# Kernel optimization log

Hardware: AMD Instinct MI355X
Metric: run time of the kernel (lower is better)

## Reference

```python
import jax, jax.numpy as jnp
import numpy as np

DIM = 512
HEADS = 16
HEAD_DIM = DIM // HEADS
WH, WW = 7, 7
N = WH * WW
OUP = 512
SCALE = HEAD_DIM ** -0.5
NW = 64  # windows per image (mask leading dim)


def _relative_position_index():
    coords = np.stack(np.meshgrid(np.arange(WH), np.arange(WW), indexing='ij'))  # (2,Wh,Ww)
    flat = coords.reshape(2, -1)                           # (2, N)
    rel = flat[:, :, None] - flat[:, None, :]              # (2, N, N)
    rel = rel.transpose(1, 2, 0).astype(np.int64)          # (N, N, 2)
    rel[:, :, 0] += WH - 1
    rel[:, :, 1] += WW - 1
    rel[:, :, 0] *= 2 * WW - 1
    return jnp.asarray(rel.sum(-1))                        # (N, N) int

REL_IDX = _relative_position_index()


def setup_inputs() -> dict:
    key = jax.random.key(0)
    ks = jax.random.split(key, 8)
    B_ = 4096
    x = jax.random.normal(ks[0], (B_, N, DIM), dtype=jnp.float32)
    mask = jnp.zeros((NW, N, N), dtype=jnp.float32)
    qkv_w = jax.random.normal(ks[1], (3 * DIM, DIM), dtype=jnp.float32) * (DIM ** -0.5)
    qkv_b = jax.random.normal(ks[2], (3 * DIM,), dtype=jnp.float32) * 0.02
    table = jax.random.normal(ks[3], ((2 * WH - 1) * (2 * WW - 1), HEADS), dtype=jnp.float32) * 0.02
    proj_w = jax.random.normal(ks[4], (OUP, DIM), dtype=jnp.float32) * (DIM ** -0.5)
    proj_b = jax.random.normal(ks[5], (OUP,), dtype=jnp.float32) * 0.02
    return {"x": x, "mask": mask, "qkv_w": qkv_w, "qkv_b": qkv_b,
            "table": table, "proj_w": proj_w, "proj_b": proj_b}


def reference(x, mask, qkv_w, qkv_b, table, proj_w, proj_b):
    B_, n, c = x.shape
    qkv = x @ qkv_w.T + qkv_b                               # (B_, N, 3C)
    qkv = qkv.reshape(B_, n, 3, HEADS, HEAD_DIM).transpose(2, 0, 3, 1, 4)
    q, k, v = qkv[0], qkv[1], qkv[2]                        # (B_, H, N, hd)
    q = q * SCALE
    attn = jnp.einsum('bhnd,bhmd->bhnm', q, k)              # (B_, H, N, N)
    bias = table[REL_IDX]                                   # (N, N, H) gather
    attn = attn + bias.transpose(2, 0, 1)[None]             # add rel-pos bias
    nW = mask.shape[0]
    attn = attn.reshape(B_ // nW, nW, HEADS, n, n) + mask[None, :, None]
    attn = attn.reshape(B_, HEADS, n, n)
    attn = jax.nn.softmax(attn, axis=-1)
    out = jnp.einsum('bhnm,bhmd->bhnd', attn, v)            # (B_, H, N, hd)
    out = out.transpose(0, 2, 1, 3).reshape(B_, n, c)
    return out @ proj_w.T + proj_b
```

## Files before the change

kernel.cpp:

```cpp
#include <hip/hip_runtime.h>
#include <hip/hip_bf16.h>
#include <stdint.h>

#define DIMC 512
#define HEADS 16
#define HEAD_DIM 32
#define NTOK 49
#define SCALE 0.17677669529663687f

typedef unsigned short u16;
typedef short bf16x8 __attribute__((ext_vector_type(8)));
typedef float f32x4 __attribute__((ext_vector_type(4)));
typedef u16 u16x8 __attribute__((ext_vector_type(8)));

#define MFMA16(a, b, c) __builtin_amdgcn_mfma_f32_16x16x32_bf16((a), (b), (c), 0, 0, 0)

__device__ __forceinline__ u16 f2bf(float f) {
  __hip_bfloat16 h = __float2bfloat16(f);
  u16 u;
  __builtin_memcpy(&u, &h, 2);
  return u;
}

__device__ __forceinline__ void gld16(const void* g, void* l) {
  __builtin_amdgcn_global_load_lds(
      (const __attribute__((address_space(1))) uint32_t*)g,
      (__attribute__((address_space(3))) uint32_t*)l, 16, 0, 0);
}

__global__ void cvt_f32_bf16(const float* __restrict__ in, u16* __restrict__ out, int n) {
  const int stride = gridDim.x * blockDim.x;
  for (int i = blockIdx.x * blockDim.x + threadIdx.x; i * 8 < n; i += stride) {
    const float4 v0 = ((const float4*)(in + i * 8))[0];
    const float4 v1 = ((const float4*)(in + i * 8))[1];
    u16x8 r;
    r[0] = f2bf(v0.x); r[1] = f2bf(v0.y); r[2] = f2bf(v0.z); r[3] = f2bf(v0.w);
    r[4] = f2bf(v1.x); r[5] = f2bf(v1.y); r[6] = f2bf(v1.z); r[7] = f2bf(v1.w);
    *(u16x8*)(out + i * 8) = r;
  }
}

__global__ void biasmask_kernel(const float* __restrict__ table, const float* __restrict__ mask,
                                float* __restrict__ bm) {
  const int wm = blockIdx.x >> 4;
  const int h  = blockIdx.x & 15;
  for (int e = threadIdx.x; e < 4096; e += 256) {
    const int r = e & 3, lane = (e >> 2) & 63, fj = (e >> 8) & 3, fi = e >> 10;
    const int row = fi * 16 + (lane >> 4) * 4 + r;
    const int col = fj * 16 + (lane & 15);
    float v;
    if (row < NTOK && col < NTOK) {
      const int yi = row / 7, xi = row % 7, yj = col / 7, xj = col % 7;
      const int idx = (yi - yj + 6) * 13 + (xi - xj + 6);
      v = table[idx * HEADS + h] + mask[wm * (NTOK * NTOK) + row * NTOK + col];
    } else {
      v = -1e30f;
    }
    bm[(size_t)blockIdx.x * 4096 + e] = v;
  }
}

template<bool A_F32, bool OUT_BF16, bool QKV_SCALE>
__global__ void gemm_tn(const void* __restrict__ Ap, const u16* __restrict__ Bp,
                        const float* __restrict__ bias, void* __restrict__ Cp,
                        int M, int N, int K, int nxt) {
  __shared__ u16 As[128 * 64];
  __shared__ u16 Bs[128 * 64];
  const int t = threadIdx.x;
  const int lane = t & 63;
  const int q = gridDim.x >> 3;
  const int l = (blockIdx.x & 7) * q + (blockIdx.x >> 3);
  const int bm0 = (l / nxt) * 128;
  const int bn0 = (l % nxt) * 128;
  const int wv = t >> 6, wr = wv >> 1, wc = wv & 1;
  const int lr = lane & 15, lg = lane >> 4;

  f32x4 acc[4][4] = {};

  int soff[4];
#pragma unroll
  for (int k = 0; k < 4; ++k) {
    const int c = t + 256 * k;
    const int row = c >> 3, sub = c & 7;
    soff[k] = ((sub ^ (row & 7)) * 8);
  }

  const int arow = t >> 1;
  const int acb  = (t & 1) * 32;

  const int nK = K >> 6;
  for (int kt = 0; kt < nK; ++kt) {
    const int k0 = kt << 6;
    __syncthreads();
#pragma unroll
    for (int k = 0; k < 4; ++k) {
      const int c = t + 256 * k;
      const int row = c >> 3;
      gld16(Bp + (size_t)(bn0 + row) * K + k0 + soff[k], Bs + c * 8);
      if (!A_F32)
        gld16((const u16*)Ap + (size_t)(bm0 + row) * K + k0 + soff[k], As + c * 8);
    }
    if (A_F32) {
      const float* A = (const float*)Ap;
      const float* src = A + (size_t)(bm0 + arow) * K + k0 + acb;
      float4 v[8];
#pragma unroll
      for (int c = 0; c < 8; ++c) v[c] = ((const float4*)src)[c];
      u16* dst = &As[arow * 64];
#pragma unroll
      for (int cc = 0; cc < 4; ++cc) {
        bf16x8 p;
        p[0] = f2bf(v[2 * cc].x); p[1] = f2bf(v[2 * cc].y);
        p[2] = f2bf(v[2 * cc].z); p[3] = f2bf(v[2 * cc].w);
        p[4] = f2bf(v[2 * cc + 1].x); p[5] = f2bf(v[2 * cc + 1].y);
        p[6] = f2bf(v[2 * cc + 1].z); p[7] = f2bf(v[2 * cc + 1].w);
        const int chunk = (acb >> 3) + cc;
        *(bf16x8*)&dst[(chunk ^ (arow & 7)) << 3] = p;
      }
    }
    __syncthreads();

#pragma unroll
    for (int kk = 0; kk < 2; ++kk) {
      bf16x8 af[4], bfr[4];
#pragma unroll
      for (int i = 0; i < 4; ++i) {
        const int row = wr * 64 + i * 16 + lr;
        af[i] = *(const bf16x8*)&As[row * 64 + (((kk * 4 + lg) ^ (row & 7)) << 3)];
      }
#pragma unroll
      for (int j = 0; j < 4; ++j) {
        const int row = wc * 64 + j * 16 + lr;
        bfr[j] = *(const bf16x8*)&Bs[row * 64 + (((kk * 4 + lg) ^ (row & 7)) << 3)];
      }
#pragma unroll
      for (int i = 0; i < 4; ++i)
#pragma unroll
        for (int j = 0; j < 4; ++j)
          acc[i][j] = MFMA16(af[i], bfr[j], acc[i][j]);
    }
  }

#pragma unroll
  for (int j = 0; j < 4; ++j) {
    const int col = bn0 + wc * 64 + j * 16 + lr;
    const float bv = bias[col];
    const float sc = (QKV_SCALE && col < DIMC) ? SCALE : 1.0f;
#pragma unroll
    for (int i = 0; i < 4; ++i) {
      const int row0 = bm0 + wr * 64 + i * 16 + lg * 4;
#pragma unroll
      for (int r = 0; r < 4; ++r) {
        const float val = (acc[i][j][r] + bv) * sc;
        if (OUT_BF16)
          ((u16*)Cp)[(size_t)(row0 + r) * N + col] = f2bf(val);
        else
          ((float*)Cp)[(size_t)(row0 + r) * N + col] = val;
      }
    }
  }
}

__global__ void attn_win(const u16* __restrict__ qkv, const float* __restrict__ bmfrag,
                         u16* __restrict__ aout) {
  __shared__ u16 P[4][64 * 64];
  __shared__ u16 Vs[4][64 * 40];
  const int t = threadIdx.x, lane = t & 63, wv = t >> 6;
  const int lr = lane & 15, lg = lane >> 4;
  const int w = blockIdx.x >> 2;
  const int h = ((blockIdx.x & 3) << 2) + wv;
  const size_t base = (size_t)w * NTOK * 1536 + h * HEAD_DIM;

  const float* bmp = bmfrag + (((size_t)(w & 63) * 16 + h) << 12);
  f32x4 s[4][4];
#pragma unroll
  for (int i = 0; i < 4; ++i)
#pragma unroll
    for (int j = 0; j < 4; ++j)
      s[i][j] = *(const f32x4*)&bmp[((i * 4 + j) * 64 + lane) * 4];

  const bf16x8 zf = {};
  bf16x8 qf[4], kf[4];
#pragma unroll
  for (int i = 0; i < 4; ++i) {
    const int row = i * 16 + lr;
    const size_t roff = base + (size_t)row * 1536 + lg * 8;
    qf[i] = (row < NTOK) ? *(const bf16x8*)&qkv[roff] : zf;
    kf[i] = (row < NTOK) ? *(const bf16x8*)&qkv[roff + DIMC] : zf;
  }

  u16x8 vreg[4];
  const u16x8 vz = {};
#pragma unroll
  for (int it = 0; it < 4; ++it) {
    const int k = it * 16 + (lane >> 2);
    const int seg = lane & 3;
    vreg[it] = (k < NTOK) ? *(const u16x8*)&qkv[base + 2 * DIMC + (size_t)k * 1536 + seg * 8]
                          : vz;
  }

  __builtin_amdgcn_s_setprio(1);
#pragma unroll
  for (int i = 0; i < 4; ++i)
#pragma unroll
    for (int j = 0; j < 4; ++j)
      s[i][j] = MFMA16(qf[i], kf[j], s[i][j]);
  __builtin_amdgcn_s_setprio(0);

  u16* Vsw = &Vs[wv][0];
#pragma unroll
  for (int it = 0; it < 4; ++it) {
    const int k = it * 16 + (lane >> 2);
    const int seg = lane & 3;
    *(u16x8*)&Vsw[k * 40 + seg * 8] = vreg[it];
  }

  u16* Pw = &P[wv][0];
#pragma unroll
  for (int i = 0; i < 4; ++i)
#pragma unroll
    for (int r = 0; r < 4; ++r) {
      const int ii = i * 16 + lg * 4 + r;
#pragma unroll
      for (int j = 0; j < 4; ++j) {
        const int jj = j * 16 + lr;
        Pw[ii * 64 + (((jj >> 3) ^ (ii & 7)) << 3) + (jj & 7)] = f2bf(__expf(s[i][j][r]));
      }
    }

  bf16x8 ones;
#pragma unroll
  for (int e = 0; e < 8; ++e) ones[e] = (short)0x3F80;
  f32x4 o[4][2] = {};
  f32x4 osum[4] = {};
#pragma unroll
  for (int ks = 0; ks < 2; ++ks) {
    bf16x8 vf[2];
#pragma unroll
    for (int dn = 0; dn < 2; ++dn) {
#pragma unroll
      for (int e = 0; e < 8; ++e) {
        const int kk = ks * 32 + lg * 8 + e;
        vf[dn][e] = (short)Vsw[kk * 40 + dn * 16 + lr];
      }
    }
    __builtin_amdgcn_s_setprio(1);
#pragma unroll
    for (int i = 0; i < 4; ++i) {
      const int row = i * 16 + lr;
      const bf16x8 pa = *(const bf16x8*)&Pw[row * 64 + (((ks * 4 + lg) ^ (row & 7)) << 3)];
#pragma unroll
      for (int dn = 0; dn < 2; ++dn)
        o[i][dn] = MFMA16(pa, vf[dn], o[i][dn]);
      osum[i] = MFMA16(pa, ones, osum[i]);
    }
    __builtin_amdgcn_s_setprio(0);
  }

#pragma unroll
  for (int i = 0; i < 4; ++i)
#pragma unroll
    for (int r = 0; r < 4; ++r) {
      const int row = i * 16 + lg * 4 + r;
      if (row < NTOK) {
        const float rinv = __builtin_amdgcn_rcpf(osum[i][r]);
        const size_t ob = ((size_t)w * NTOK + row) * DIMC + h * HEAD_DIM;
#pragma unroll
        for (int dn = 0; dn < 2; ++dn)
          aout[ob + dn * 16 + lr] = f2bf(o[i][dn][r] * rinv);
      }
    }
}

extern "C" void kernel_launch(void* const* d_in, const int* in_sizes, int n_in,
                              void* d_out, int out_size, void* d_ws, size_t ws_size,
                              hipStream_t stream) {
  const float* x      = (const float*)d_in[0];
  const float* mask   = (const float*)d_in[1];
  const float* qkv_w  = (const float*)d_in[2];
  const float* qkv_b  = (const float*)d_in[3];
  const float* table  = (const float*)d_in[4];
  const float* proj_w = (const float*)d_in[5];
  const float* proj_b = (const float*)d_in[6];
  float* out = (float*)d_out;

  const int M = 4096 * NTOK;

  char* ws = (char*)d_ws;
  u16*   qkv_bf   = (u16*)ws;
  u16*   wqkv_bf  = (u16*)(ws + 616562688ull);
  u16*   wproj_bf = (u16*)(ws + 618135552ull);
  float* biasmask = (float*)(ws + 618659840ull);
  u16*   attn_bf  = (u16*)(ws + 635437056ull);

  cvt_f32_bf16<<<768, 256, 0, stream>>>(qkv_w, wqkv_bf, 1536 * 512);
  cvt_f32_bf16<<<256, 256, 0, stream>>>(proj_w, wproj_bf, 512 * 512);
  biasmask_kernel<<<1024, 256, 0, stream>>>(table, mask, biasmask);

  gemm_tn<true, true, true><<<1568 * 12, 256, 0, stream>>>(
      x, wqkv_bf, qkv_b, qkv_bf, M, 1536, 512, 12);

  attn_win<<<4096 * 4, 256, 0, stream>>>(qkv_bf, biasmask, attn_bf);

  gemm_tn<false, false, false><<<1568 * 4, 256, 0, stream>>>(
      attn_bf, wproj_bf, proj_b, out, M, 512, 512, 4);
}
```

Measured before the change: 1.188 ms.

## Pre-convert x to bf16 in a separate pass and store bias-mask as bf16

Adds a standalone pass that converts the fp32 input activations to bf16, so the QKV GEMM can load its A operand with async global-to-LDS loads instead of reading fp32 and converting in registers on every tile. The GEMM is collapsed into a single bf16-only template. The precomputed bias+mask fragments are stored as bf16 instead of fp32, halving that read in the attention kernel, and the attention output buffer reuses the x_bf buffer. The trade is an extra full read and write of x (about 100M elements), plus bf16 rounding of the bias/mask values.

```diff
diff --git a/kernel.cpp b/kernel.cpp
--- a/kernel.cpp
+++ b/kernel.cpp
@@ -11,6 +11,7 @@
 typedef unsigned short u16;
 typedef short bf16x8 __attribute__((ext_vector_type(8)));
 typedef float f32x4 __attribute__((ext_vector_type(4)));
+typedef u16 u16x4 __attribute__((ext_vector_type(4)));
 typedef u16 u16x8 __attribute__((ext_vector_type(8)));
 
 #define MFMA16(a, b, c) __builtin_amdgcn_mfma_f32_16x16x32_bf16((a), (b), (c), 0, 0, 0)
@@ -20,6 +21,13 @@
   u16 u;
   __builtin_memcpy(&u, &h, 2);
   return u;
+}
+
+__device__ __forceinline__ float bf2f(u16 u) {
+  const uint32_t b = ((uint32_t)u) << 16;
+  float f;
+  __builtin_memcpy(&f, &b, 4);
+  return f;
 }
 
 __device__ __forceinline__ void gld16(const void* g, void* l) {
@@ -41,7 +49,7 @@
 }
 
 __global__ void biasmask_kernel(const float* __restrict__ table, const float* __restrict__ mask,
-                                float* __restrict__ bm) {
+                                u16* __restrict__ bm) {
   const int wm = blockIdx.x >> 4;
   const int h  = blockIdx.x & 15;
   for (int e = threadIdx.x; e < 4096; e += 256) {
@@ -56,20 +64,21 @@
     } else {
       v = -1e30f;
     }
-    bm[(size_t)blockIdx.x * 4096 + e] = v;
-  }
-}
-
-template<bool A_F32, bool OUT_BF16, bool QKV_SCALE>
-__global__ void gemm_tn(const void* __restrict__ Ap, const u16* __restrict__ Bp,
-                        const float* __restrict__ bias, void* __restrict__ Cp,
-                        int M, int N, int K, int nxt) {
+    bm[(size_t)blockIdx.x * 4096 + e] = f2bf(v);
+  }
+}
+
+template<bool OUT_BF16, bool QKV_SCALE>
+__global__ void gemm_bf16(const u16* __restrict__ Ap, const u16* __restrict__ Bp,
+                          const float* __restrict__ bias, void* __restrict__ Cp,
+                          int M, int N, int K, int nxt) {
   __shared__ u16 As[128 * 64];
   __shared__ u16 Bs[128 * 64];
   const int t = threadIdx.x;
   const int lane = t & 63;
   const int q = gridDim.x >> 3;
-  const int l = (blockIdx.x & 7) * q + (blockIdx.x >> 3);
+  const int lin = blockIdx.x;
+  const int l = (lin & 7) * q + (lin >> 3);
   const int bm0 = (l / nxt) * 128;
   const int bn0 = (l % nxt) * 128;
   const int wv = t >> 6, wr = wv >> 1, wc = wv & 1;
@@ -85,9 +94,6 @@
     soff[k] = ((sub ^ (row & 7)) * 8);
   }
 
-  const int arow = t >> 1;
-  const int acb  = (t & 1) * 32;
-
   const int nK = K >> 6;
   for (int kt = 0; kt < nK; ++kt) {
     const int k0 = kt << 6;
@@ -96,27 +102,8 @@
     for (int k = 0; k < 4; ++k) {
       const int c = t + 256 * k;
       const int row = c >> 3;
+      gld16(Ap + (size_t)(bm0 + row) * K + k0 + soff[k], As + c * 8);
       gld16(Bp + (size_t)(bn0 + row) * K + k0 + soff[k], Bs + c * 8);
-      if (!A_F32)
-        gld16((const u16*)Ap + (size_t)(bm0 + row) * K + k0 + soff[k], As + c * 8);
-    }
-    if (A_F32) {
-      const float* A = (const float*)Ap;
-      const float* src = A + (size_t)(bm0 + arow) * K + k0 + acb;
-      float4 v[8];
-#pragma unroll
-      for (int c = 0; c < 8; ++c) v[c] = ((const float4*)src)[c];
-      u16* dst = &As[arow * 64];
-#pragma unroll
-      for (int cc = 0; cc < 4; ++cc) {
-        bf16x8 p;
-        p[0] = f2bf(v[2 * cc].x); p[1] = f2bf(v[2 * cc].y);
-        p[2] = f2bf(v[2 * cc].z); p[3] = f2bf(v[2 * cc].w);
-        p[4] = f2bf(v[2 * cc + 1].x); p[5] = f2bf(v[2 * cc + 1].y);
-        p[6] = f2bf(v[2 * cc + 1].z); p[7] = f2bf(v[2 * cc + 1].w);
-        const int chunk = (acb >> 3) + cc;
-        *(bf16x8*)&dst[(chunk ^ (arow & 7)) << 3] = p;
-      }
     }
     __syncthreads();
 
@@ -161,7 +148,7 @@
   }
 }
 
-__global__ void attn_win(const u16* __restrict__ qkv, const float* __restrict__ bmfrag,
+__global__ void attn_win(const u16* __restrict__ qkv, const u16* __restrict__ bmfrag,
                          u16* __restrict__ aout) {
   __shared__ u16 P[4][64 * 64];
   __shared__ u16 Vs[4][64 * 40];
@@ -171,13 +158,16 @@
   const int h = ((blockIdx.x & 3) << 2) + wv;
   const size_t base = (size_t)w * NTOK * 1536 + h * HEAD_DIM;
 
-  const float* bmp = bmfrag + (((size_t)(w & 63) * 16 + h) << 12);
+  const u16* bmp = bmfrag + (((size_t)(w & 63) * 16 + h) << 12);
   f32x4 s[4][4];
 #pragma unroll
   for (int i = 0; i < 4; ++i)
 #pragma unroll
-    for (int j = 0; j < 4; ++j)
-      s[i][j] = *(const f32x4*)&bmp[((i * 4 + j) * 64 + lane) * 4];
+    for (int j = 0; j < 4; ++j) {
+      const u16x4 b4 = *(const u16x4*)&bmp[((i * 4 + j) * 64 + lane) * 4];
+#pragma unroll
+      for (int r = 0; r < 4; ++r) s[i][j][r] = bf2f(b4[r]);
+    }
 
   const bf16x8 zf = {};
   bf16x8 qf[4], kf[4];
@@ -290,18 +280,20 @@
   u16*   qkv_bf   = (u16*)ws;
   u16*   wqkv_bf  = (u16*)(ws + 616562688ull);
   u16*   wproj_bf = (u16*)(ws + 618135552ull);
-  float* biasmask = (float*)(ws + 618659840ull);
-  u16*   attn_bf  = (u16*)(ws + 635437056ull);
+  u16*   biasmask = (u16*)(ws + 618659840ull);
+  u16*   x_bf     = (u16*)(ws + 627048448ull);
+  u16*   attn_bf  = x_bf;
 
   cvt_f32_bf16<<<768, 256, 0, stream>>>(qkv_w, wqkv_bf, 1536 * 512);
   cvt_f32_bf16<<<256, 256, 0, stream>>>(proj_w, wproj_bf, 512 * 512);
   biasmask_kernel<<<1024, 256, 0, stream>>>(table, mask, biasmask);
-
-  gemm_tn<true, true, true><<<1568 * 12, 256, 0, stream>>>(
-      x, wqkv_bf, qkv_b, qkv_bf, M, 1536, 512, 12);
+  cvt_f32_bf16<<<1792, 256, 0, stream>>>(x, x_bf, M * DIMC);
+
+  gemm_bf16<true, true><<<1568 * 12, 256, 0, stream>>>(
+      x_bf, wqkv_bf, qkv_b, qkv_bf, M, 1536, 512, 12);
 
   attn_win<<<4096 * 4, 256, 0, stream>>>(qkv_bf, biasmask, attn_bf);
 
-  gemm_tn<false, false, false><<<1568 * 4, 256, 0, stream>>>(
+  gemm_bf16<false, false><<<1568 * 4, 256, 0, stream>>>(
       attn_bf, wproj_bf, proj_b, out, M, 512, 512, 4);
 }
```

Result: faster. 1.061 ms (-10.7%).
